# Kernel tuning notes

Measured on AMD Instinct MI355X. Metric: run time of the kernel, lower is better.

Reference implementation:

```python
import jax, jax.numpy as jnp
import numpy as np

N = 50000   # nodes
E = 800000  # edges (avg degree 16)
H = 128     # hidden_dim / emb_dim
OUT = 128   # out_dim
NUM_BOND_TYPE = 6
NUM_BOND_DIR = 6


def setup_inputs() -> dict:
    key = jax.random.key(0)
    ks = jax.random.split(key, 12)
    s = 0.05
    return {
        "x": jax.random.normal(ks[0], (N, H), jnp.float32),
        "edge_index": jax.random.randint(ks[1], (2, E), 0, N),
        "edge_attr": jax.random.randint(ks[2], (E, 2), 0, 6),
        "prelu_a": jnp.float32(0.25),  # PReLU single shared slope (torch default)
        "W_enc": jax.random.normal(ks[3], (H, H), jnp.float32) * s,  # enc_to_dec, no bias
        "edge_emb1": jax.random.normal(ks[4], (NUM_BOND_TYPE, H), jnp.float32) * s,
        "edge_emb2": jax.random.normal(ks[5], (NUM_BOND_DIR, H), jnp.float32) * s,
        "W1": jax.random.normal(ks[6], (H, 2 * H), jnp.float32) * s,
        "b1": jnp.zeros((2 * H,), jnp.float32),
        "W2": jax.random.normal(ks[7], (2 * H, OUT), jnp.float32) * s,
        "b2": jnp.zeros((OUT,), jnp.float32),
    }


def reference(x, edge_index, edge_attr, prelu_a, W_enc, edge_emb1, edge_emb2, W1, b1, W2, b2):
    n = x.shape[0]
    # GNNDecoder: PReLU then enc_to_dec linear (no bias)
    x = jnp.where(x > 0, x, prelu_a * x)
    x = x @ W_enc

    # GINConv.forward: add self loops, self-loop edge_attr = [5, 0]
    loop = jnp.arange(n)
    src = jnp.concatenate([edge_index[0], loop])  # [E+N]
    dst = jnp.concatenate([edge_index[1], loop])  # [E+N]
    ea1 = jnp.concatenate([edge_attr[:, 0], jnp.full((n,), 5, edge_attr.dtype)])
    ea2 = jnp.concatenate([edge_attr[:, 1], jnp.zeros((n,), edge_attr.dtype)])

    # edge embedding lookup + gather-add message + scatter-add aggregate
    edge_emb = edge_emb1[ea1] + edge_emb2[ea2]          # [E+N, H]
    msg = x[src] + edge_emb                             # message(x_j, edge_attr)
    agg = jax.ops.segment_sum(msg, dst, num_segments=n)  # aggr='add'

    # update: MLP Linear(H,2H) -> SiLU -> Linear(2H,OUT)
    h = jax.nn.silu(agg @ W1 + b1)
    return h @ W2 + b2
```

## Files before the change

kernel.cpp:

```cpp
#include <hip/hip_runtime.h>

typedef unsigned short u16;
typedef unsigned int   u32;
typedef __attribute__((ext_vector_type(8))) short short8;
typedef __attribute__((ext_vector_type(4))) float f32x4;

__device__ __forceinline__ float bl(u32 u){ union{u32 i; float f;} c; c.i = u << 16; return c.f; }
__device__ __forceinline__ float bh(u32 u){ union{u32 i; float f;} c; c.i = u & 0xffff0000u; return c.f; }
__device__ __forceinline__ u16 f2b(float f){
  union{float f; u32 i;} c; c.f = f;
  return (u16)((c.i + 0x8000u) >> 16);
}
__device__ __forceinline__ u32 pk2(float a, float b){
  union{float f; u32 i;} x, y; x.f = a; y.f = b;
  return ((x.i + 0x8000u) >> 16) | ((y.i + 0x8000u) & 0xffff0000u);
}

__device__ __forceinline__ void wave_scan_bsum(
    const int* __restrict__ bsum, int nb, int* __restrict__ sPre, int t)
{
  int carry = 0;
  for (int c0 = 0; c0 < nb; c0 += 64) {
    int idx = c0 + t;
    int b = (idx < nb) ? bsum[idx] : 0;
    int v = b;
    #pragma unroll
    for (int d = 1; d < 64; d <<= 1) {
      int u = __shfl_up(v, d);
      if (t >= d) v += u;
    }
    if (idx < nb) sPre[idx] = carry + v - b;
    carry += __shfl(v, 63);
  }
}

__global__ __launch_bounds__(256) void k_enc_count(
    const float* __restrict__ x, const float* __restrict__ pa,
    const float* __restrict__ Wenc, u16* __restrict__ xencQ, int N,
    const int* __restrict__ ei, int* __restrict__ cnt,
    int* __restrict__ rank, int E, int encBlocks)
{
  if ((int)blockIdx.x >= encBlocks) {
    int e = ((int)blockIdx.x - encBlocks) * 256 + threadIdx.x;
    if (e < E) rank[e] = atomicAdd(&cnt[ei[E + e]], 1);
    return;
  }

  const int SK = 136, NT = 8;
  __shared__ u16 sB[128 * SK];

  const int t = threadIdx.x;
  for (int j = 0; j < 64; j++) {
    int i = t + 256 * j;
    int k = i >> 7, n = i & 127;
    sB[n * SK + k] = f2b(Wenc[i]);
  }
  __syncthreads();

  const float slope = pa[0];
  const int lane = t & 63, wave = t >> 6, quad = lane >> 4, l16 = lane & 15;
  const int m0 = blockIdx.x * 128 + wave * 32;
  if (m0 >= N) return;

  f32x4 acc[2][NT];
  #pragma unroll
  for (int mr = 0; mr < 2; mr++)
    #pragma unroll
    for (int nt = 0; nt < NT; nt++) acc[mr][nt] = (f32x4){0.f, 0.f, 0.f, 0.f};

  #pragma unroll
  for (int ks = 0; ks < 4; ks++) {
    const int k0 = ks * 32 + quad * 8;
    union { u32 u[4]; short8 s; } a[2];
    #pragma unroll
    for (int mr = 0; mr < 2; mr++) {
      int row = m0 + mr * 16 + l16; row = min(row, N - 1);
      const float4* ap = (const float4*)&x[(size_t)row * 128 + k0];
      float4 f0 = ap[0], f1 = ap[1];
      float v0 = f0.x > 0.f ? f0.x : slope * f0.x;
      float v1 = f0.y > 0.f ? f0.y : slope * f0.y;
      float v2 = f0.z > 0.f ? f0.z : slope * f0.z;
      float v3 = f0.w > 0.f ? f0.w : slope * f0.w;
      float v4 = f1.x > 0.f ? f1.x : slope * f1.x;
      float v5 = f1.y > 0.f ? f1.y : slope * f1.y;
      float v6 = f1.z > 0.f ? f1.z : slope * f1.z;
      float v7 = f1.w > 0.f ? f1.w : slope * f1.w;
      a[mr].u[0] = pk2(v0, v1); a[mr].u[1] = pk2(v2, v3);
      a[mr].u[2] = pk2(v4, v5); a[mr].u[3] = pk2(v6, v7);
    }
    #pragma unroll
    for (int nt = 0; nt < NT; nt++) {
      short8 b = *(const short8*)&sB[(nt * 16 + l16) * SK + k0];
      acc[0][nt] = __builtin_amdgcn_mfma_f32_16x16x32_bf16(a[0].s, b, acc[0][nt], 0, 0, 0);
      acc[1][nt] = __builtin_amdgcn_mfma_f32_16x16x32_bf16(a[1].s, b, acc[1][nt], 0, 0, 0);
    }
  }

  #pragma unroll
  for (int mr = 0; mr < 2; mr++)
    #pragma unroll
    for (int nt = 0; nt < NT; nt++) {
      int col = nt * 16 + l16;
      int q = col >> 5, cq = col & 31;
      #pragma unroll
      for (int r = 0; r < 4; r++) {
        int row = m0 + mr * 16 + quad * 4 + r;
        if (row < N)
          xencQ[((size_t)q * N + row) * 32 + cq] = f2b(acc[mr][nt][r]);
      }
    }
}

__global__ __launch_bounds__(256) void k_scanW(
    const int* __restrict__ cnt, int* __restrict__ offs,
    int* __restrict__ bsum, int n, int nb,
    const float* __restrict__ W1, const float* __restrict__ W2,
    const float* __restrict__ e1, const float* __restrict__ e2,
    u16* __restrict__ W1T, u16* __restrict__ W2T, u32* __restrict__ embP)
{
  if ((int)blockIdx.x >= nb) {
    int i = ((int)blockIdx.x - nb) * 256 + threadIdx.x;
    if (i < 32768) {
      int nn = i >> 7, k = i & 127;
      W1T[i] = f2b(W1[k * 256 + nn]);
    } else if (i < 65536) {
      int j = i - 32768;
      int nn = j >> 8, k = j & 255;
      W2T[j] = f2b(W2[k * 128 + nn]);
    } else {
      int j = i - 65536;
      int q = j / 576, rem = j - q * 576;
      int c = rem >> 4, s = rem & 15;
      int c1 = c / 6, c2 = c - c1 * 6;
      int col = q * 32 + s * 2;
      embP[j] = pk2(e1[c1 * 128 + col]     + e2[c2 * 128 + col],
                    e1[c1 * 128 + col + 1] + e2[c2 * 128 + col + 1]);
    }
    return;
  }

  __shared__ int sS[256];
  const int b = blockIdx.x, t = threadIdx.x;
  const int i0 = b * 1024 + t * 4;
  int4 v = make_int4(0, 0, 0, 0);
  if (i0 + 3 < n) v = *(const int4*)&cnt[i0];
  else {
    if (i0     < n) v.x = cnt[i0];
    if (i0 + 1 < n) v.y = cnt[i0 + 1];
    if (i0 + 2 < n) v.z = cnt[i0 + 2];
  }
  int s = v.x + v.y + v.z + v.w;
  sS[t] = s;
  __syncthreads();
  for (int d = 1; d < 256; d <<= 1) {
    int val = (t >= d) ? sS[t - d] : 0;
    __syncthreads();
    sS[t] += val;
    __syncthreads();
  }
  int ex = sS[t] - s;
  if (t == 255) bsum[b] = sS[t];
  int o0 = ex, o1 = o0 + v.x, o2 = o1 + v.y, o3 = o2 + v.z;
  if (i0     < n) offs[i0]     = o0;
  if (i0 + 1 < n) offs[i0 + 1] = o1;
  if (i0 + 2 < n) offs[i0 + 2] = o2;
  if (i0 + 3 < n) offs[i0 + 3] = o3;
}

__global__ __launch_bounds__(256) void k_fill(
    const int* __restrict__ ei, const int* __restrict__ ea,
    const int* __restrict__ offs, const int* __restrict__ rank,
    const int* __restrict__ bsum, int nb,
    u32* __restrict__ recs, int E)
{
  __shared__ int sPre[256];
  const int t = threadIdx.x;
  if (t < 64) wave_scan_bsum(bsum, nb, sPre, t);
  __syncthreads();

  int e = blockIdx.x * 256 + t;
  if (e >= E) return;
  int src = ei[e];
  int dst = ei[E + e];
  int2 a = *(const int2*)&ea[2 * e];
  int pos = offs[dst] + sPre[dst >> 10] + rank[e];
  recs[pos] = (u32)src | ((u32)(a.x * 6 + a.y) << 26);
}

struct B8 { uint2 x[8]; u32 r[8]; };

__device__ __forceinline__ void issue8(B8& b, u32 rv, int grp,
                                       const u32* __restrict__ xq, int sub) {
  #pragma unroll
  for (int k = 0; k < 8; k++) {
    u32 r = __shfl(rv, grp + k);
    b.r[k] = r;
    b.x[k] = *(const uint2*)&xq[(size_t)(r & 0x3ffffffu) * 16 + sub * 2];
  }
}

__device__ __forceinline__ void acc8(float* a, const B8& b,
                                     const u32* __restrict__ sEq,
                                     int sub, int dleft) {
  #pragma unroll
  for (int k = 0; k < 8; k++) {
    if (k < dleft) {
      uint2 e = *(const uint2*)&sEq[(b.r[k] >> 26) * 18 + sub * 2];
      uint2 x = b.x[k];
      a[0] += bl(x.x) + bl(e.x);  a[1] += bh(x.x) + bh(e.x);
      a[2] += bl(x.y) + bl(e.y);  a[3] += bh(x.y) + bh(e.y);
    }
  }
}

__global__ __launch_bounds__(256, 4) void k_gather(
    const int* __restrict__ offs, const int* __restrict__ bsum, int nb,
    const u32* __restrict__ recs, const u32* __restrict__ embP,
    const u32* __restrict__ xencQ, u32* __restrict__ aggbQ, int N, int E)
{
  const int ES = 18;
  __shared__ u32 sE[4 * 36 * ES];
  __shared__ int sPre[256];

  const int t = threadIdx.x;
  for (int i = t; i < 4 * 36 * 16; i += 256) {
    int qc = i >> 4, s = i & 15;
    sE[qc * ES + s] = embP[i];
  }
  if (t < 64) wave_scan_bsum(bsum, nb, sPre, t);
  __syncthreads();

  const int lane = t & 63, wave = t >> 6;
  const int grp = lane & 56, sub = lane & 7;
  const int v = blockIdx.x * 32 + wave * 8 + (lane >> 3);
  const bool vok = v < N;
  const int vc = vok ? v : N - 1;
  const int beg = offs[vc] + sPre[vc >> 10];
  const int end = (vc == N - 1) ? E : (offs[vc + 1] + sPre[(vc + 1) >> 10]);
  const int d = vok ? end - beg : 0;

  u32 rv0 = 0, rv1 = 0, rv2 = 0, rv3 = 0;
  if (d > 0)  rv0 = recs[min(beg + sub, end - 1)];
  if (d > 8)  rv1 = recs[min(beg + 8 + sub, end - 1)];
  if (d > 16) rv2 = recs[min(beg + 16 + sub, end - 1)];
  if (d > 24) rv3 = recs[min(beg + 24 + sub, end - 1)];

  #pragma unroll 1
  for (int q = 0; q < 4; q++) {
    const u32* xq = xencQ + (size_t)q * N * 16;
    const u32* sEq = &sE[q * 36 * ES];

    uint2 xs = *(const uint2*)&xq[(size_t)vc * 16 + sub * 2];
    uint2 es = *(const uint2*)&sEq[30 * ES + sub * 2];
    float a[4];
    a[0] = bl(xs.x) + bl(es.x);  a[1] = bh(xs.x) + bh(es.x);
    a[2] = bl(xs.y) + bl(es.y);  a[3] = bh(xs.y) + bh(es.y);

    if (d > 0) {
      B8 bA, bB;
      issue8(bA, rv0, grp, xq, sub);
      if (d > 8) issue8(bB, rv1, grp, xq, sub);
      acc8(a, bA, sEq, sub, d);
      if (d > 8) {
        if (d > 16) issue8(bA, rv2, grp, xq, sub);
        acc8(a, bB, sEq, sub, d - 8);
        if (d > 16) {
          if (d > 24) issue8(bB, rv3, grp, xq, sub);
          acc8(a, bA, sEq, sub, d - 16);
          if (d > 24) {
            acc8(a, bB, sEq, sub, d - 24);
            for (int j0 = 32; j0 < d; j0 += 8) {
              u32 rvt = recs[min(beg + j0 + sub, end - 1)];
              issue8(bA, rvt, grp, xq, sub);
              acc8(a, bA, sEq, sub, d - j0);
            }
          }
        }
      }
    }

    if (vok) {
      uint2 o;
      o.x = pk2(a[0], a[1]);
      o.y = pk2(a[2], a[3]);
      *(uint2*)&aggbQ[((size_t)q * N + vc) * 16 + sub * 2] = o;
    }
  }
}

__global__ __launch_bounds__(256) void k_mlp(
    const u16* __restrict__ aggbQ, const u16* __restrict__ W1T,
    const float* __restrict__ b1, const u16* __restrict__ W2T,
    const float* __restrict__ b2, float* __restrict__ out, int N)
{
  const int SK = 136;
  __shared__ u16 sW[128 * SK];
  __shared__ u16 sH[128 * SK];
  __shared__ float sB1[256];
  __shared__ float sB2[128];

  const int t = threadIdx.x;
  const int lane = t & 63, wave = t >> 6, quad = lane >> 4, l16 = lane & 15;
  const int m0 = blockIdx.x * 128 + wave * 32;

  if (t < 128) sB2[t] = b2[t];
  sB1[t] = b1[t];

  union { uint4 q; short8 s; } a[2][4];
  #pragma unroll
  for (int mr = 0; mr < 2; mr++) {
    int row = min(m0 + mr * 16 + l16, N - 1);
    #pragma unroll
    for (int ks = 0; ks < 4; ks++)
      a[mr][ks].q = *(const uint4*)&aggbQ[((size_t)ks * N + row) * 32 + quad * 8];
  }

  f32x4 acc2[2][8];
  #pragma unroll
  for (int mr = 0; mr < 2; mr++)
    #pragma unroll
    for (int nt = 0; nt < 8; nt++) acc2[mr][nt] = (f32x4){0.f, 0.f, 0.f, 0.f};

  for (int half = 0; half < 2; half++) {
    #pragma unroll
    for (int j = 0; j < 8; j++) {
      int i = t + 256 * j;
      int n = i >> 4, k8 = i & 15;
      *(uint4*)&sW[n * SK + k8 * 8] =
          *(const uint4*)&W1T[(size_t)(half * 128 + n) * 128 + k8 * 8];
    }
    __syncthreads();

    f32x4 acc1[2][8];
    #pragma unroll
    for (int mr = 0; mr < 2; mr++)
      #pragma unroll
      for (int nt = 0; nt < 8; nt++) acc1[mr][nt] = (f32x4){0.f, 0.f, 0.f, 0.f};

    #pragma unroll
    for (int ks = 0; ks < 4; ks++) {
      const int k0 = ks * 32 + quad * 8;
      #pragma unroll
      for (int nt = 0; nt < 8; nt++) {
        short8 b = *(const short8*)&sW[(nt * 16 + l16) * SK + k0];
        acc1[0][nt] = __builtin_amdgcn_mfma_f32_16x16x32_bf16(a[0][ks].s, b, acc1[0][nt], 0, 0, 0);
        acc1[1][nt] = __builtin_amdgcn_mfma_f32_16x16x32_bf16(a[1][ks].s, b, acc1[1][nt], 0, 0, 0);
      }
    }

    #pragma unroll
    for (int mr = 0; mr < 2; mr++)
      #pragma unroll
      for (int nt = 0; nt < 8; nt++) {
        int col = nt * 16 + l16;
        float bias = sB1[half * 128 + col];
        #pragma unroll
        for (int r = 0; r < 4; r++) {
          float z = acc1[mr][nt][r] + bias;
          float s = z / (1.f + __expf(-z));
          sH[(wave * 32 + mr * 16 + quad * 4 + r) * SK + col] = f2b(s);
        }
      }
    __syncthreads();

    #pragma unroll
    for (int j = 0; j < 8; j++) {
      int i = t + 256 * j;
      int n = i >> 4, k8 = i & 15;
      *(uint4*)&sW[n * SK + k8 * 8] =
          *(const uint4*)&W2T[(size_t)n * 256 + half * 128 + k8 * 8];
    }
    __syncthreads();

    #pragma unroll
    for (int ks = 0; ks < 4; ks++) {
      const int k0 = ks * 32 + quad * 8;
      union { uint4 q; short8 s; } ah[2];
      #pragma unroll
      for (int mr = 0; mr < 2; mr++)
        ah[mr].q = *(const uint4*)&sH[(wave * 32 + mr * 16 + l16) * SK + k0];
      #pragma unroll
      for (int nt = 0; nt < 8; nt++) {
        short8 b = *(const short8*)&sW[(nt * 16 + l16) * SK + k0];
        acc2[0][nt] = __builtin_amdgcn_mfma_f32_16x16x32_bf16(ah[0].s, b, acc2[0][nt], 0, 0, 0);
        acc2[1][nt] = __builtin_amdgcn_mfma_f32_16x16x32_bf16(ah[1].s, b, acc2[1][nt], 0, 0, 0);
      }
    }
    __syncthreads();
  }

  #pragma unroll
  for (int mr = 0; mr < 2; mr++)
    #pragma unroll
    for (int nt = 0; nt < 8; nt++) {
      int col = nt * 16 + l16;
      float bias = sB2[col];
      #pragma unroll
      for (int r = 0; r < 4; r++) {
        int row = m0 + mr * 16 + quad * 4 + r;
        if (row < N) out[(size_t)row * 128 + col] = acc2[mr][nt][r] + bias;
      }
    }
}

extern "C" void kernel_launch(void* const* d_in, const int* in_sizes, int n_in,
                              void* d_out, int out_size, void* d_ws, size_t ws_size,
                              hipStream_t stream) {
  const float* x    = (const float*)d_in[0];
  const int*   ei   = (const int*)d_in[1];
  const int*   ea   = (const int*)d_in[2];
  const float* pa   = (const float*)d_in[3];
  const float* Wenc = (const float*)d_in[4];
  const float* e1   = (const float*)d_in[5];
  const float* e2   = (const float*)d_in[6];
  const float* W1   = (const float*)d_in[7];
  const float* b1   = (const float*)d_in[8];
  const float* W2   = (const float*)d_in[9];
  const float* b2   = (const float*)d_in[10];
  float* out = (float*)d_out;

  const int N = in_sizes[0] / 128;
  const int E = in_sizes[1] / 2;

  char* ws = (char*)d_ws;
  size_t off = 0;
  auto alloc = [&](size_t bytes) {
    void* p = ws + off;
    off = (off + bytes + 255) & ~(size_t)255;
    return p;
  };
  u16*   xencQ  = (u16*)  alloc((size_t)N * 128 * 2);
  u32*   aggbQ  = (u32*)  alloc((size_t)N * 64 * 4);
  int*   cnt    = (int*)  alloc((size_t)N * 4);
  int*   offs   = (int*)  alloc((size_t)(N + 1) * 4);
  int*   rank   = (int*)  alloc((size_t)E * 4);
  int*   bsum   = (int*)  alloc(256 * 4);
  u32*   recs   = (u32*)  alloc((size_t)(E + 64) * 4);
  u16*   W1T    = (u16*)  alloc(256 * 128 * 2);
  u16*   W2T    = (u16*)  alloc(128 * 256 * 2);
  u32*   embP   = (u32*)  alloc(2304 * 4);

  const int encBlocks    = (N + 127) / 128;
  const int edgeBlocks   = (E + 255) / 256;
  const int nb           = (N + 1023) / 1024;
  const int gatherBlocks = (N + 31) / 32;

  hipMemsetAsync(cnt, 0, (size_t)N * 4, stream);
  k_enc_count<<<encBlocks + edgeBlocks, 256, 0, stream>>>(
      x, pa, Wenc, xencQ, N, ei, cnt, rank, E, encBlocks);
  k_scanW<<<nb + 265, 256, 0, stream>>>(
      cnt, offs, bsum, N, nb, W1, W2, e1, e2, W1T, W2T, embP);
  k_fill<<<edgeBlocks, 256, 0, stream>>>(ei, ea, offs, rank, bsum, nb, recs, E);
  k_gather<<<gatherBlocks, 256, 0, stream>>>(
      offs, bsum, nb, recs, embP, (const u32*)xencQ, aggbQ, N, E);
  k_mlp<<<encBlocks, 256, 0, stream>>>(
      (const u16*)aggbQ, W1T, b1, W2T, b2, out, N);
}
```

Baseline: 224.0 us.

## Pretranspose weights in prep kernel, drop rank array, persistent quarter-synced gather

A new prep kernel transposes Wenc, W1 and W2 to bf16 through shared-memory tiles and zeroes the count array, which replaces the memset and the uncoalesced per-element transposes. The edge counting no longer stores a per-edge rank. The fill kernel instead claims slots with a decrementing atomic on the counts and also writes final offsets, so gather no longer rescans the block sums. Gather becomes a persistent 2048-block kernel that processes one feature quarter at a time across all nodes, with a spin-wait grid barrier between quarters to keep each quarter's slice cache-resident. The barrier assumes all blocks are co-resident, and it gives up after a fixed iteration count, which risks ordering problems. The decrementing atomics also make edge order within each node nondeterministic.

```diff
diff --git a/kernel.cpp b/kernel.cpp
--- a/kernel.cpp
+++ b/kernel.cpp
@@ -34,15 +34,80 @@
   }
 }
 
+__device__ __forceinline__ void tr_tile(
+    const float* __restrict__ in, int K, int Nn, u16* __restrict__ out,
+    int k0, int n0, int t, u16* __restrict__ sT )
+{
+  #pragma unroll
+  for (int rr = 0; rr < 4; rr++) {
+    int row = (t >> 4) + rr * 16;
+    int c4  = (t & 15) * 4;
+    float4 v = *(const float4*)&in[(size_t)(k0 + row) * Nn + n0 + c4];
+    sT[(c4 + 0) * 72 + row] = f2b(v.x);
+    sT[(c4 + 1) * 72 + row] = f2b(v.y);
+    sT[(c4 + 2) * 72 + row] = f2b(v.z);
+    sT[(c4 + 3) * 72 + row] = f2b(v.w);
+  }
+  __syncthreads();
+  #pragma unroll
+  for (int ww = 0; ww < 2; ww++) {
+    int nn = (t >> 3) + ww * 32;
+    int c8 = (t & 7) * 8;
+    uint4 val = *(const uint4*)&sT[nn * 72 + c8];
+    *(uint4*)&out[(size_t)(n0 + nn) * K + k0 + c8] = val;
+  }
+}
+
+__global__ __launch_bounds__(256) void k_prep(
+    const float* __restrict__ Wenc, const float* __restrict__ W1,
+    const float* __restrict__ W2, const float* __restrict__ e1,
+    const float* __restrict__ e2, u16* __restrict__ WencT,
+    u16* __restrict__ W1T, u16* __restrict__ W2T,
+    u32* __restrict__ embP, int* __restrict__ cnt, int* __restrict__ bar,
+    int N)
+{
+  __shared__ u16 sT[64 * 72];
+  const int b = blockIdx.x, t = threadIdx.x;
+
+  if (b < 4) {
+    tr_tile(Wenc, 128, 128, WencT, (b & 1) * 64, (b >> 1) * 64, t, sT);
+  } else if (b < 12) {
+    int l = b - 4;
+    tr_tile(W1, 128, 256, W1T, (l & 1) * 64, (l >> 1) * 64, t, sT);
+  } else if (b < 20) {
+    int l = b - 12;
+    tr_tile(W2, 256, 128, W2T, (l & 3) * 64, (l >> 2) * 64, t, sT);
+  } else if (b == 20) {
+    if (t < 4) bar[t] = 0;
+    for (int i = t; i < 2304; i += 256) {
+      int q = i / 576, rem = i - q * 576;
+      int c = rem >> 4, s = rem & 15;
+      int c1 = c / 6, c2 = c - c1 * 6;
+      int col = q * 32 + s * 2;
+      embP[i] = pk2(e1[c1 * 128 + col]     + e2[c2 * 128 + col],
+                    e1[c1 * 128 + col + 1] + e2[c2 * 128 + col + 1]);
+    }
+  } else {
+    int base = (b - 21) * 1024 + t * 4;
+    if (base + 3 < N) *(int4*)&cnt[base] = make_int4(0, 0, 0, 0);
+    else {
+      if (base     < N) cnt[base]     = 0;
+      if (base + 1 < N) cnt[base + 1] = 0;
+      if (base + 2 < N) cnt[base + 2] = 0;
+      if (base + 3 < N) cnt[base + 3] = 0;
+    }
+  }
+}
+
 __global__ __launch_bounds__(256) void k_enc_count(
     const float* __restrict__ x, const float* __restrict__ pa,
-    const float* __restrict__ Wenc, u16* __restrict__ xencQ, int N,
+    const u16* __restrict__ WT, u16* __restrict__ xencQ, int N,
     const int* __restrict__ ei, int* __restrict__ cnt,
-    int* __restrict__ rank, int E, int encBlocks)
+    int E, int encBlocks)
 {
   if ((int)blockIdx.x >= encBlocks) {
     int e = ((int)blockIdx.x - encBlocks) * 256 + threadIdx.x;
-    if (e < E) rank[e] = atomicAdd(&cnt[ei[E + e]], 1);
+    if (e < E) atomicAdd(&cnt[ei[E + e]], 1);
     return;
   }
 
@@ -50,10 +115,11 @@
   __shared__ u16 sB[128 * SK];
 
   const int t = threadIdx.x;
-  for (int j = 0; j < 64; j++) {
+  #pragma unroll
+  for (int j = 0; j < 8; j++) {
     int i = t + 256 * j;
-    int k = i >> 7, n = i & 127;
-    sB[n * SK + k] = f2b(Wenc[i]);
+    int n = i >> 4, k8 = i & 15;
+    *(uint4*)&sB[n * SK + k8 * 8] = *(const uint4*)&WT[n * 128 + k8 * 8];
   }
   __syncthreads();
 
@@ -111,34 +177,10 @@
     }
 }
 
-__global__ __launch_bounds__(256) void k_scanW(
+__global__ __launch_bounds__(256) void k_scan(
     const int* __restrict__ cnt, int* __restrict__ offs,
-    int* __restrict__ bsum, int n, int nb,
-    const float* __restrict__ W1, const float* __restrict__ W2,
-    const float* __restrict__ e1, const float* __restrict__ e2,
-    u16* __restrict__ W1T, u16* __restrict__ W2T, u32* __restrict__ embP)
-{
-  if ((int)blockIdx.x >= nb) {
-    int i = ((int)blockIdx.x - nb) * 256 + threadIdx.x;
-    if (i < 32768) {
-      int nn = i >> 7, k = i & 127;
-      W1T[i] = f2b(W1[k * 256 + nn]);
-    } else if (i < 65536) {
-      int j = i - 32768;
-      int nn = j >> 8, k = j & 255;
-      W2T[j] = f2b(W2[k * 128 + nn]);
-    } else {
-      int j = i - 65536;
-      int q = j / 576, rem = j - q * 576;
-      int c = rem >> 4, s = rem & 15;
-      int c1 = c / 6, c2 = c - c1 * 6;
-      int col = q * 32 + s * 2;
-      embP[j] = pk2(e1[c1 * 128 + col]     + e2[c2 * 128 + col],
-                    e1[c1 * 128 + col + 1] + e2[c2 * 128 + col + 1]);
-    }
-    return;
-  }
-
+    int* __restrict__ bsum, int n)
+{
   __shared__ int sS[256];
   const int b = blockIdx.x, t = threadIdx.x;
   const int i0 = b * 1024 + t * 4;
@@ -169,22 +211,35 @@
 
 __global__ __launch_bounds__(256) void k_fill(
     const int* __restrict__ ei, const int* __restrict__ ea,
-    const int* __restrict__ offs, const int* __restrict__ rank,
+    const int* __restrict__ offs, int* __restrict__ cnt,
     const int* __restrict__ bsum, int nb,
-    u32* __restrict__ recs, int E)
+    u32* __restrict__ recs, int* __restrict__ offsF, int E, int N,
+    int edgeBlocks)
 {
   __shared__ int sPre[256];
   const int t = threadIdx.x;
   if (t < 64) wave_scan_bsum(bsum, nb, sPre, t);
   __syncthreads();
+
+  if ((int)blockIdx.x >= edgeBlocks) {
+    int base = ((int)blockIdx.x - edgeBlocks) * 1024 + t * 4;
+    #pragma unroll
+    for (int j = 0; j < 4; j++) {
+      int i = base + j;
+      if (i < N) offsF[i] = offs[i] + sPre[i >> 10];
+      else if (i == N) offsF[i] = E;
+    }
+    return;
+  }
 
   int e = blockIdx.x * 256 + t;
   if (e >= E) return;
   int src = ei[e];
   int dst = ei[E + e];
   int2 a = *(const int2*)&ea[2 * e];
-  int pos = offs[dst] + sPre[dst >> 10] + rank[e];
-  recs[pos] = (u32)src | ((u32)(a.x * 6 + a.y) << 26);
+  int r = atomicAdd(&cnt[dst], -1);
+  int end = (dst == N - 1) ? E : (offs[dst + 1] + sPre[(dst + 1) >> 10]);
+  recs[end - r] = (u32)src | ((u32)(a.x * 6 + a.y) << 26);
 }
 
 struct B8 { uint2 x[8]; u32 r[8]; };
@@ -213,77 +268,88 @@
   }
 }
 
-__global__ __launch_bounds__(256, 4) void k_gather(
-    const int* __restrict__ offs, const int* __restrict__ bsum, int nb,
-    const u32* __restrict__ recs, const u32* __restrict__ embP,
-    const u32* __restrict__ xencQ, u32* __restrict__ aggbQ, int N, int E)
+__global__ __launch_bounds__(256, 8) void k_gather(
+    const int* __restrict__ offsF, const u32* __restrict__ recs,
+    const u32* __restrict__ embP, const u32* __restrict__ xencQ,
+    u32* __restrict__ aggbQ, int* __restrict__ bar, int N, int nTiles)
 {
   const int ES = 18;
-  __shared__ u32 sE[4 * 36 * ES];
-  __shared__ int sPre[256];
+  __shared__ u32 sE[144 * ES];
 
   const int t = threadIdx.x;
-  for (int i = t; i < 4 * 36 * 16; i += 256) {
-    int qc = i >> 4, s = i & 15;
-    sE[qc * ES + s] = embP[i];
-  }
-  if (t < 64) wave_scan_bsum(bsum, nb, sPre, t);
+  for (int i = t; i < 2304; i += 256)
+    sE[(i >> 4) * ES + (i & 15)] = embP[i];
   __syncthreads();
 
   const int lane = t & 63, wave = t >> 6;
   const int grp = lane & 56, sub = lane & 7;
-  const int v = blockIdx.x * 32 + wave * 8 + (lane >> 3);
-  const bool vok = v < N;
-  const int vc = vok ? v : N - 1;
-  const int beg = offs[vc] + sPre[vc >> 10];
-  const int end = (vc == N - 1) ? E : (offs[vc + 1] + sPre[(vc + 1) >> 10]);
-  const int d = vok ? end - beg : 0;
-
-  u32 rv0 = 0, rv1 = 0, rv2 = 0, rv3 = 0;
-  if (d > 0)  rv0 = recs[min(beg + sub, end - 1)];
-  if (d > 8)  rv1 = recs[min(beg + 8 + sub, end - 1)];
-  if (d > 16) rv2 = recs[min(beg + 16 + sub, end - 1)];
-  if (d > 24) rv3 = recs[min(beg + 24 + sub, end - 1)];
-
-  #pragma unroll 1
+
   for (int q = 0; q < 4; q++) {
     const u32* xq = xencQ + (size_t)q * N * 16;
     const u32* sEq = &sE[q * 36 * ES];
 
-    uint2 xs = *(const uint2*)&xq[(size_t)vc * 16 + sub * 2];
-    uint2 es = *(const uint2*)&sEq[30 * ES + sub * 2];
-    float a[4];
-    a[0] = bl(xs.x) + bl(es.x);  a[1] = bh(xs.x) + bh(es.x);
-    a[2] = bl(xs.y) + bl(es.y);  a[3] = bh(xs.y) + bh(es.y);
-
-    if (d > 0) {
-      B8 bA, bB;
-      issue8(bA, rv0, grp, xq, sub);
-      if (d > 8) issue8(bB, rv1, grp, xq, sub);
-      acc8(a, bA, sEq, sub, d);
-      if (d > 8) {
-        if (d > 16) issue8(bA, rv2, grp, xq, sub);
-        acc8(a, bB, sEq, sub, d - 8);
-        if (d > 16) {
-          if (d > 24) issue8(bB, rv3, grp, xq, sub);
-          acc8(a, bA, sEq, sub, d - 16);
-          if (d > 24) {
-            acc8(a, bB, sEq, sub, d - 24);
-            for (int j0 = 32; j0 < d; j0 += 8) {
-              u32 rvt = recs[min(beg + j0 + sub, end - 1)];
-              issue8(bA, rvt, grp, xq, sub);
-              acc8(a, bA, sEq, sub, d - j0);
+    for (int tile = blockIdx.x; tile < nTiles; tile += gridDim.x) {
+      const int v = tile * 32 + wave * 8 + (lane >> 3);
+      const bool vok = v < N;
+      const int vc = vok ? v : N - 1;
+      const int beg = offsF[vc];
+      const int end = offsF[vc + 1];
+      const int d = vok ? end - beg : 0;
+
+      u32 rv0 = 0, rv1 = 0, rv2 = 0, rv3 = 0;
+      if (d > 0)  rv0 = recs[min(beg + sub, end - 1)];
+      if (d > 8)  rv1 = recs[min(beg + 8 + sub, end - 1)];
+      if (d > 16) rv2 = recs[min(beg + 16 + sub, end - 1)];
+      if (d > 24) rv3 = recs[min(beg + 24 + sub, end - 1)];
+
+      uint2 xs = *(const uint2*)&xq[(size_t)vc * 16 + sub * 2];
+      uint2 es = *(const uint2*)&sEq[30 * ES + sub * 2];
+      float a[4];
+      a[0] = bl(xs.x) + bl(es.x);  a[1] = bh(xs.x) + bh(es.x);
+      a[2] = bl(xs.y) + bl(es.y);  a[3] = bh(xs.y) + bh(es.y);
+
+      if (d > 0) {
+        B8 bA, bB;
+        issue8(bA, rv0, grp, xq, sub);
+        if (d > 8) issue8(bB, rv1, grp, xq, sub);
+        acc8(a, bA, sEq, sub, d);
+        if (d > 8) {
+          if (d > 16) issue8(bA, rv2, grp, xq, sub);
+          acc8(a, bB, sEq, sub, d - 8);
+          if (d > 16) {
+            if (d > 24) issue8(bB, rv3, grp, xq, sub);
+            acc8(a, bA, sEq, sub, d - 16);
+            if (d > 24) {
+              acc8(a, bB, sEq, sub, d - 24);
+              for (int j0 = 32; j0 < d; j0 += 8) {
+                u32 rvt = recs[min(beg + j0 + sub, end - 1)];
+                issue8(bA, rvt, grp, xq, sub);
+                acc8(a, bA, sEq, sub, d - j0);
+              }
             }
           }
         }
       }
-    }
-
-    if (vok) {
-      uint2 o;
-      o.x = pk2(a[0], a[1]);
-      o.y = pk2(a[2], a[3]);
-      *(uint2*)&aggbQ[((size_t)q * N + vc) * 16 + sub * 2] = o;
+
+      if (vok) {
+        uint2 o;
+        o.x = pk2(a[0], a[1]);
+        o.y = pk2(a[2], a[3]);
+        *(uint2*)&aggbQ[((size_t)q * N + vc) * 16 + sub * 2] = o;
+      }
+    }
+
+    if (q < 3) {
+      __syncthreads();
+      if (t == 0) {
+        __hip_atomic_fetch_add(&bar[q], 1, __ATOMIC_RELAXED,
+                               __HIP_MEMORY_SCOPE_AGENT);
+        int it = 0;
+        while (__hip_atomic_load(&bar[q], __ATOMIC_RELAXED,
+                                 __HIP_MEMORY_SCOPE_AGENT) < (int)gridDim.x
+               && it < 10000) it++;
+      }
+      __syncthreads();
     }
   }
 }
@@ -433,26 +499,31 @@
   u32*   aggbQ  = (u32*)  alloc((size_t)N * 64 * 4);
   int*   cnt    = (int*)  alloc((size_t)N * 4);
   int*   offs   = (int*)  alloc((size_t)(N + 1) * 4);
-  int*   rank   = (int*)  alloc((size_t)E * 4);
+  int*   offsF  = (int*)  alloc((size_t)(N + 1) * 4);
   int*   bsum   = (int*)  alloc(256 * 4);
   u32*   recs   = (u32*)  alloc((size_t)(E + 64) * 4);
+  u16*   WencT  = (u16*)  alloc(128 * 128 * 2);
   u16*   W1T    = (u16*)  alloc(256 * 128 * 2);
   u16*   W2T    = (u16*)  alloc(128 * 256 * 2);
   u32*   embP   = (u32*)  alloc(2304 * 4);
-
-  const int encBlocks    = (N + 127) / 128;
-  const int edgeBlocks   = (E + 255) / 256;
-  const int nb           = (N + 1023) / 1024;
-  const int gatherBlocks = (N + 31) / 32;
-
-  hipMemsetAsync(cnt, 0, (size_t)N * 4, stream);
+  int*   bar    = (int*)  alloc(256);
+
+  const int encBlocks   = (N + 127) / 128;
+  const int edgeBlocks  = (E + 255) / 256;
+  const int nb          = (N + 1023) / 1024;
+  const int nTiles      = (N + 31) / 32;
+  const int riderBlocks = (N + 1024) / 1024;
+  const int prepBlocks  = 21 + (N + 1023) / 1024;
+
+  k_prep<<<prepBlocks, 256, 0, stream>>>(Wenc, W1, W2, e1, e2,
+                                         WencT, W1T, W2T, embP, cnt, bar, N);
   k_enc_count<<<encBlocks + edgeBlocks, 256, 0, stream>>>(
-      x, pa, Wenc, xencQ, N, ei, cnt, rank, E, encBlocks);
-  k_scanW<<<nb + 265, 256, 0, stream>>>(
-      cnt, offs, bsum, N, nb, W1, W2, e1, e2, W1T, W2T, embP);
-  k_fill<<<edgeBlocks, 256, 0, stream>>>(ei, ea, offs, rank, bsum, nb, recs, E);
-  k_gather<<<gatherBlocks, 256, 0, stream>>>(
-      offs, bsum, nb, recs, embP, (const u32*)xencQ, aggbQ, N, E);
+      x, pa, WencT, xencQ, N, ei, cnt, E, encBlocks);
+  k_scan<<<nb, 256, 0, stream>>>(cnt, offs, bsum, N);
+  k_fill<<<edgeBlocks + riderBlocks, 256, 0, stream>>>(
+      ei, ea, offs, cnt, bsum, nb, recs, offsF, E, N, edgeBlocks);
+  k_gather<<<2048, 256, 0, stream>>>(
+      offsF, recs, embP, (const u32*)xencQ, aggbQ, bar, N, nTiles);
   k_mlp<<<encBlocks, 256, 0, stream>>>(
       (const u16*)aggbQ, W1T, b1, W2T, b2, out, N);
 }
```

After: 751.8 us. 236% more time.
